# Optimization experiments

Measured on AMD Instinct MI355X. Metric: run time of the kernel, lower is better.

Reference implementation:

```python
import jax, jax.numpy as jnp
import numpy as np

MARGIN = 0.1

def setup_inputs() -> dict:
    key = jax.random.key(0)
    k1, k2 = jax.random.split(key)
    embeddings = jax.random.normal(k1, (8192, 128), dtype=jnp.float32)
    labels = jax.random.randint(k2, (8192,), 0, 64, dtype=jnp.int64)
    return {"embeddings": embeddings, "labels": labels}

def reference(embeddings, labels):
    # sim[i,j] = <e_i, e_j>
    sim = embeddings @ embeddings.T  # [n, n]
    eq = labels[:, None] == labels[None, :]  # pos mask (includes diagonal)
    # per entry: exp(margin - sim) for positives, exp(sim - margin) for negatives
    terms = jnp.where(eq, jnp.exp(MARGIN - sim), jnp.exp(sim - MARGIN))
    # loss_i = log(sum_j terms[i,j]); loss = mean_i loss_i
    return jnp.mean(jnp.log(jnp.sum(terms, axis=1)))
```

## Files before the change

kernel.cpp:

```cpp
#include <hip/hip_runtime.h>
#include <hip/hip_bf16.h>

#define N 8192
#define D 128
#define LOG2E  1.44269504088896f
#define LN2    0.69314718055995f
#define COLSB  272

typedef __attribute__((ext_vector_type(8))) short bf16x8;
typedef __attribute__((ext_vector_type(4))) float f32x4;

#if __has_builtin(__builtin_amdgcn_exp2f)
#define EXP2(x) __builtin_amdgcn_exp2f(x)
#else
#define EXP2(x) exp2f(x)
#endif
#if __has_builtin(__builtin_amdgcn_logf)
#define LOG2(x) __builtin_amdgcn_logf(x)
#else
#define LOG2(x) log2f(x)
#endif

static __device__ __forceinline__ unsigned short f2bf(float f) {
    union { float f; unsigned int u; } x;
    x.f = f;
    unsigned int r = ((x.u >> 16) & 1u) + 0x7FFFu;
    return (unsigned short)((x.u + r) >> 16);
}

__global__ void prep_kernel(const float* __restrict__ E,
                            unsigned short* __restrict__ Eb,
                            unsigned int* __restrict__ counter) {
    int idx = blockIdx.x * 256 + threadIdx.x;
    float4 v = ((const float4*)E)[idx];
    ushort4 o;
    o.x = f2bf(v.x); o.y = f2bf(v.y); o.z = f2bf(v.z); o.w = f2bf(v.w);
    ((ushort4*)Eb)[idx] = o;
    if (idx == 0) *counter = 0u;
}

__global__ __launch_bounds__(256) void fused_kernel(
        const unsigned short* __restrict__ Eb,
        const int* __restrict__ labels,
        float* __restrict__ part) {
    __shared__ __align__(16) char aA[128 * COLSB];
    __shared__ __align__(16) char bB[128 * COLSB];
    __shared__ int   labC[128];
    __shared__ int   labR[128];
    __shared__ float colacc[128];

    const int tid  = threadIdx.x;
    const int wid  = tid >> 6;
    const int lane = tid & 63;
    const int q = lane >> 4;
    const int l = lane & 15;

    const int b = blockIdx.x;
    int r = (int)(64.5f - sqrtf(64.5f * 64.5f - 2.0f * (float)b));
    while ((r + 1) * 64 - ((r + 1) * r) / 2 <= b) ++r;
    while (r * 64 - (r * (r - 1)) / 2 > b) --r;
    const int c = r + (b - (r * 64 - (r * (r - 1)) / 2));
    const bool diag = (r == c);
    const int tile_m0 = r * 128;
    const int n_begin = c * 128;
    const int mrow0 = wid * 32;

    const char* gA = (const char*)Eb + (size_t)tile_m0 * 256;
    const char* gB = (const char*)Eb + (size_t)n_begin * 256;
    const int lrow_st = (tid >> 4);
    const int loff_st = (tid & 15) * 16;
#pragma unroll
    for (int i = 0; i < 16; ++i) {
        float4 v = *(const float4*)(gA + i * 4096 + tid * 16);
        *(float4*)(aA + (i * 16 + lrow_st) * COLSB + loff_st) = v;
    }
    if (!diag) {
#pragma unroll
        for (int i = 0; i < 16; ++i) {
            float4 v = *(const float4*)(gB + i * 4096 + tid * 16);
            *(float4*)(bB + (i * 16 + lrow_st) * COLSB + loff_st) = v;
        }
    }
    if (tid < 128) { labC[tid] = labels[n_begin + tid]; colacc[tid] = 0.0f; }
    else           { labR[tid - 128] = labels[tile_m0 + (tid - 128)]; }
    __syncthreads();

    const char* bBp = diag ? aA : bB;

    bf16x8 a[2][4];
#pragma unroll
    for (int g = 0; g < 2; ++g)
#pragma unroll
        for (int kk = 0; kk < 4; ++kk)
            a[g][kk] = *(const bf16x8*)(aA + (mrow0 + g * 16 + l) * COLSB + kk * 64 + q * 16);

    int lrow[8];
#pragma unroll
    for (int g = 0; g < 2; ++g)
#pragma unroll
        for (int rr = 0; rr < 4; ++rr)
            lrow[g * 4 + rr] = labR[mrow0 + g * 16 + q * 4 + rr];

    float sum[8];
#pragma unroll
    for (int i = 0; i < 8; ++i) sum[i] = 0.0f;

#pragma clang loop unroll(disable)
    for (int s = 0; s < 8; ++s) {
        const int lc = labC[s * 16 + l];
        const char* lb = bBp + (s * 16 + l) * COLSB + q * 16;
        bf16x8 b0 = *(const bf16x8*)(lb);
        bf16x8 b1 = *(const bf16x8*)(lb + 64);
        bf16x8 b2 = *(const bf16x8*)(lb + 128);
        bf16x8 b3 = *(const bf16x8*)(lb + 192);

        f32x4 acc0 = (f32x4){0.f, 0.f, 0.f, 0.f};
        f32x4 acc1 = (f32x4){0.f, 0.f, 0.f, 0.f};
        acc0 = __builtin_amdgcn_mfma_f32_16x16x32_bf16(a[0][0], b0, acc0, 0, 0, 0);
        acc0 = __builtin_amdgcn_mfma_f32_16x16x32_bf16(a[0][1], b1, acc0, 0, 0, 0);
        acc0 = __builtin_amdgcn_mfma_f32_16x16x32_bf16(a[0][2], b2, acc0, 0, 0, 0);
        acc0 = __builtin_amdgcn_mfma_f32_16x16x32_bf16(a[0][3], b3, acc0, 0, 0, 0);
        acc1 = __builtin_amdgcn_mfma_f32_16x16x32_bf16(a[1][0], b0, acc1, 0, 0, 0);
        acc1 = __builtin_amdgcn_mfma_f32_16x16x32_bf16(a[1][1], b1, acc1, 0, 0, 0);
        acc1 = __builtin_amdgcn_mfma_f32_16x16x32_bf16(a[1][2], b2, acc1, 0, 0, 0);
        acc1 = __builtin_amdgcn_mfma_f32_16x16x32_bf16(a[1][3], b3, acc1, 0, 0, 0);

        float cp = 0.0f;
#pragma unroll
        for (int g = 0; g < 2; ++g) {
#pragma unroll
            for (int rr = 0; rr < 4; ++rr) {
                float sv = (g == 0) ? acc0[rr] : acc1[rr];
                bool eq = (lrow[g * 4 + rr] == lc);
                float cc = eq ? -LOG2E : LOG2E;
                float term = EXP2(cc * (sv - 0.1f));
                sum[g * 4 + rr] += term;
                cp += term;
            }
        }
        if (!diag) {
            cp += __shfl_xor(cp, 16);
            cp += __shfl_xor(cp, 32);
            if (q == 0) atomicAdd(&colacc[s * 16 + l], cp);
        }
    }

#pragma unroll
    for (int i = 0; i < 8; ++i) {
        float v = sum[i];
        v += __shfl_xor(v, 1);
        v += __shfl_xor(v, 2);
        v += __shfl_xor(v, 4);
        v += __shfl_xor(v, 8);
        sum[i] = v;
    }
    if (l == 0) {
#pragma unroll
        for (int g = 0; g < 2; ++g)
#pragma unroll
            for (int rr = 0; rr < 4; ++rr)
                part[(size_t)c * N + tile_m0 + mrow0 + g * 16 + q * 4 + rr] = sum[g * 4 + rr];
    }

    __syncthreads();
    if (!diag && tid < 128)
        part[(size_t)r * N + n_begin + tid] = colacc[tid];
}

__global__ void finalize_kernel(const float* __restrict__ part,
                                float* __restrict__ bpart,
                                unsigned int* __restrict__ counter,
                                float* __restrict__ out) {
    __shared__ float red[4];
    __shared__ unsigned int tk;
    const int tid = threadIdx.x;
    const int i = blockIdx.x * 256 + tid;

    float s = 0.0f;
#pragma unroll 8
    for (int x = 0; x < 64; ++x) s += part[(size_t)x * N + i];
    float v = LOG2(s) * LN2;
#pragma unroll
    for (int off = 1; off <= 32; off <<= 1) v += __shfl_xor(v, off);
    if ((tid & 63) == 0) red[tid >> 6] = v;
    __syncthreads();
    if (tid == 0) {
        bpart[blockIdx.x] = red[0] + red[1] + red[2] + red[3];
        __threadfence();
        tk = atomicAdd(counter, 1u);
    }
    __syncthreads();
    if (tk == 31u) {
        __threadfence();
        if (tid < 64) {
            float t = (tid < 32)
                ? __hip_atomic_load(&bpart[tid], __ATOMIC_RELAXED,
                                    __HIP_MEMORY_SCOPE_AGENT)
                : 0.0f;
#pragma unroll
            for (int off = 1; off <= 32; off <<= 1) t += __shfl_xor(t, off);
            if (tid == 0) out[0] = t * (1.0f / (float)N);
        }
    }
}

extern "C" void kernel_launch(void* const* d_in, const int* in_sizes, int n_in,
                              void* d_out, int out_size, void* d_ws, size_t ws_size,
                              hipStream_t stream) {
    const float* E = (const float*)d_in[0];
    const int* labels = (const int*)d_in[1];
    float* out = (float*)d_out;

    unsigned short* Eb = (unsigned short*)d_ws;
    float* part = (float*)((char*)d_ws + (size_t)N * D * 2);
    float* bpart = part + (size_t)64 * N;
    unsigned int* counter = (unsigned int*)(bpart + 32);

    prep_kernel<<<1024, 256, 0, stream>>>(E, Eb, counter);
    fused_kernel<<<2080, 256, 0, stream>>>(Eb, labels, part);
    finalize_kernel<<<32, 256, 0, stream>>>(part, bpart, counter, out);
}
```

Before: 98.83 us.

## Pre-swizzle bf16 embeddings into MFMA fragment layout and load operands directly from global

The prep kernel now writes bf16 embeddings in an MFMA-fragment-ordered layout so that each lane's 16-byte operand chunk is contiguous across the wavefront. The fused kernel drops the two 128x272-byte LDS tiles and loads A and B fragments directly from global memory with coalesced 16-byte loads. This removes the LDS staging traffic and sharply cuts LDS usage, which can raise occupancy. In exchange, B fragments are re-read from global/L2 by all four waves of each block instead of being shared through LDS, and loads now sit inside the loop without explicit prefetch.

New measurement: 83.75 us. -15.3%, faster.

```diff
diff --git a/kernel.cpp b/kernel.cpp
--- a/kernel.cpp
+++ b/kernel.cpp
@@ -5,7 +5,6 @@
 #define D 128
 #define LOG2E  1.44269504088896f
 #define LN2    0.69314718055995f
-#define COLSB  272
 
 typedef __attribute__((ext_vector_type(8))) short bf16x8;
 typedef __attribute__((ext_vector_type(4))) float f32x4;
@@ -29,22 +28,28 @@
 }
 
 __global__ void prep_kernel(const float* __restrict__ E,
-                            unsigned short* __restrict__ Eb,
+                            uint4* __restrict__ Eb2,
                             unsigned int* __restrict__ counter) {
-    int idx = blockIdx.x * 256 + threadIdx.x;
-    float4 v = ((const float4*)E)[idx];
-    ushort4 o;
-    o.x = f2bf(v.x); o.y = f2bf(v.y); o.z = f2bf(v.z); o.w = f2bf(v.w);
-    ((ushort4*)Eb)[idx] = o;
-    if (idx == 0) *counter = 0u;
+    const int j = blockIdx.x * 256 + threadIdx.x;
+    const int l  = j & 15;
+    const int q  = (j >> 4) & 3;
+    const int kk = (j >> 6) & 3;
+    const int S  = j >> 8;
+    const float4* src = (const float4*)(E + (size_t)(S * 16 + l) * D + kk * 32 + q * 8);
+    float4 f0 = src[0], f1 = src[1];
+    uint4 o;
+    o.x = f2bf(f0.x) | ((unsigned)f2bf(f0.y) << 16);
+    o.y = f2bf(f0.z) | ((unsigned)f2bf(f0.w) << 16);
+    o.z = f2bf(f1.x) | ((unsigned)f2bf(f1.y) << 16);
+    o.w = f2bf(f1.z) | ((unsigned)f2bf(f1.w) << 16);
+    Eb2[j] = o;
+    if (j == 0) *counter = 0u;
 }
 
 __global__ __launch_bounds__(256) void fused_kernel(
-        const unsigned short* __restrict__ Eb,
+        const unsigned short* __restrict__ Eb2,
         const int* __restrict__ labels,
         float* __restrict__ part) {
-    __shared__ __align__(16) char aA[128 * COLSB];
-    __shared__ __align__(16) char bB[128 * COLSB];
     __shared__ int   labC[128];
     __shared__ int   labR[128];
     __shared__ float colacc[128];
@@ -65,35 +70,21 @@
     const int n_begin = c * 128;
     const int mrow0 = wid * 32;
 
-    const char* gA = (const char*)Eb + (size_t)tile_m0 * 256;
-    const char* gB = (const char*)Eb + (size_t)n_begin * 256;
-    const int lrow_st = (tid >> 4);
-    const int loff_st = (tid & 15) * 16;
-#pragma unroll
-    for (int i = 0; i < 16; ++i) {
-        float4 v = *(const float4*)(gA + i * 4096 + tid * 16);
-        *(float4*)(aA + (i * 16 + lrow_st) * COLSB + loff_st) = v;
-    }
-    if (!diag) {
-#pragma unroll
-        for (int i = 0; i < 16; ++i) {
-            float4 v = *(const float4*)(gB + i * 4096 + tid * 16);
-            *(float4*)(bB + (i * 16 + lrow_st) * COLSB + loff_st) = v;
-        }
-    }
+    const char* base = (const char*)Eb2;
+
+    bf16x8 a[2][4];
+#pragma unroll
+    for (int g = 0; g < 2; ++g) {
+        const char* pa = base + (size_t)(r * 8 + wid * 2 + g) * 4096 + lane * 16;
+#pragma unroll
+        for (int kk = 0; kk < 4; ++kk)
+            a[g][kk] = *(const bf16x8*)(pa + kk * 1024);
+    }
+
     if (tid < 128) { labC[tid] = labels[n_begin + tid]; colacc[tid] = 0.0f; }
     else           { labR[tid - 128] = labels[tile_m0 + (tid - 128)]; }
     __syncthreads();
 
-    const char* bBp = diag ? aA : bB;
-
-    bf16x8 a[2][4];
-#pragma unroll
-    for (int g = 0; g < 2; ++g)
-#pragma unroll
-        for (int kk = 0; kk < 4; ++kk)
-            a[g][kk] = *(const bf16x8*)(aA + (mrow0 + g * 16 + l) * COLSB + kk * 64 + q * 16);
-
     int lrow[8];
 #pragma unroll
     for (int g = 0; g < 2; ++g)
@@ -107,12 +98,12 @@
 
 #pragma clang loop unroll(disable)
     for (int s = 0; s < 8; ++s) {
+        const char* pb = base + (size_t)(c * 8 + s) * 4096 + lane * 16;
+        bf16x8 b0 = *(const bf16x8*)(pb);
+        bf16x8 b1 = *(const bf16x8*)(pb + 1024);
+        bf16x8 b2 = *(const bf16x8*)(pb + 2048);
+        bf16x8 b3 = *(const bf16x8*)(pb + 3072);
         const int lc = labC[s * 16 + l];
-        const char* lb = bBp + (s * 16 + l) * COLSB + q * 16;
-        bf16x8 b0 = *(const bf16x8*)(lb);
-        bf16x8 b1 = *(const bf16x8*)(lb + 64);
-        bf16x8 b2 = *(const bf16x8*)(lb + 128);
-        bf16x8 b3 = *(const bf16x8*)(lb + 192);
 
         f32x4 acc0 = (f32x4){0.f, 0.f, 0.f, 0.f};
         f32x4 acc1 = (f32x4){0.f, 0.f, 0.f, 0.f};
@@ -211,12 +202,12 @@
     const int* labels = (const int*)d_in[1];
     float* out = (float*)d_out;
 
-    unsigned short* Eb = (unsigned short*)d_ws;
+    unsigned short* Eb2 = (unsigned short*)d_ws;
     float* part = (float*)((char*)d_ws + (size_t)N * D * 2);
     float* bpart = part + (size_t)64 * N;
     unsigned int* counter = (unsigned int*)(bpart + 32);
 
-    prep_kernel<<<1024, 256, 0, stream>>>(E, Eb, counter);
-    fused_kernel<<<2080, 256, 0, stream>>>(Eb, labels, part);
+    prep_kernel<<<512, 256, 0, stream>>>(E, (uint4*)Eb2, counter);
+    fused_kernel<<<2080, 256, 0, stream>>>(Eb2, labels, part);
     finalize_kernel<<<32, 256, 0, stream>>>(part, bpart, counter, out);
 }
```
